# Optimization experiments

Hardware: AMD Instinct MI355X
Metric: run time of the kernel (lower is better)

Reference implementation:

```python
import jax, jax.numpy as jnp
import numpy as np

ALPHA_MIN = 1e-6
SN_EPS = 1e-6


def _spectral_normalize(W, u):
    # One power iteration (torch spectral_norm, n_power_iterations=1).
    v = W.T @ u
    v = v / (jnp.linalg.norm(v) + SN_EPS)
    u1 = W @ v
    u1 = u1 / (jnp.linalg.norm(u1) + SN_EPS)
    u1 = jax.lax.stop_gradient(u1)
    v = jax.lax.stop_gradient(v)
    sigma = u1 @ (W @ v)
    return W / sigma


def setup_inputs() -> dict:
    key = jax.random.key(0)
    ks = jax.random.split(key, 11)
    B, T, D, K = 32, 2048, 512, 128
    x = jax.random.normal(ks[0], (B, T, D), jnp.float32)
    dt = jax.random.uniform(ks[1], (B, T), jnp.float32)
    alpha_mod = jax.random.normal(ks[2], (B, T, K), jnp.float32)
    omega_mod = jax.random.normal(ks[3], (B, T, K), jnp.float32)
    tau_mod = jax.random.normal(ks[4], (B, T, 1), jnp.float32)
    s_real_raw = jax.random.normal(ks[5], (K,), jnp.float32)
    s_imag = jax.random.normal(ks[6], (K,), jnp.float32)
    tau_raw = jax.random.normal(ks[7], (1,), jnp.float32)
    W_orig = jax.random.normal(ks[8], (K, D), jnp.float32) * (1.0 / np.sqrt(D))
    b = jax.random.normal(ks[9], (K,), jnp.float32) * 0.01
    u_sn = jax.random.normal(ks[10], (K,), jnp.float32)
    u_sn = u_sn / jnp.linalg.norm(u_sn)
    return {"x": x, "dt": dt, "alpha_mod": alpha_mod, "omega_mod": omega_mod,
            "tau_mod": tau_mod, "s_real_raw": s_real_raw, "s_imag": s_imag,
            "tau_raw": tau_raw, "W_orig": W_orig, "b": b, "u_sn": u_sn}


def reference(x, dt, alpha_mod, omega_mod, tau_mod, s_real_raw, s_imag,
              tau_raw, W_orig, b, u_sn):
    B, T, D = x.shape
    K = W_orig.shape[0]

    # global timescale and poles
    tau = jax.nn.softplus(tau_raw[0]) + 1e-3
    alpha0 = (jax.nn.softplus(s_real_raw) + ALPHA_MIN) * tau  # [K]
    omega0 = s_imag * tau                                      # [K]

    # time-varying modulation (all log-scale)
    scale = jnp.exp(tau_mod)                                   # [B,T,1]
    alpha = alpha0 * jnp.exp(alpha_mod) * scale                # [B,T,K]
    omega = omega0 * jnp.exp(omega_mod) * scale                # [B,T,K]

    dt3 = dt[..., None]                                        # [B,T,1]
    rho = jnp.exp(-alpha * dt3)                                # [B,T,K]
    theta = omega * dt3
    cos_t = jnp.cos(theta)
    sin_t = jnp.sin(theta)

    # spectral-norm projection u = x @ W_sn^T + b -> [B,T,K]
    W_sn = _spectral_normalize(W_orig, u_sn)
    u = jnp.einsum('btd,kd->btk', x, W_sn) + b

    # complex recurrence: z_t = rho_t * e^{i theta_t} * z_{t-1} + u_t
    def step(carry, inp):
        c, s = carry
        rt, ct, st, ut = inp
        c_new = rt * (c * ct - s * st) + ut
        s_new = rt * (c * st + s * ct)
        return (c_new, s_new), (c_new, s_new)

    xs = (jnp.swapaxes(rho, 0, 1), jnp.swapaxes(cos_t, 0, 1),
          jnp.swapaxes(sin_t, 0, 1), jnp.swapaxes(u, 0, 1))  # [T,B,K]
    init = (jnp.zeros((B, K), u.dtype), jnp.zeros((B, K), u.dtype))
    _, (C, S) = jax.lax.scan(step, init, xs)
    C = jnp.swapaxes(C, 0, 1)  # [B,T,K]
    S = jnp.swapaxes(S, 0, 1)
    return jnp.concatenate([C, S], axis=-1)  # [B,T,2K]
```

## Files before the change

### kernel.cpp

```cpp
#include <hip/hip_runtime.h>
#include <hip/hip_bf16.h>
#include <math.h>

typedef __bf16 bf16x8 __attribute__((ext_vector_type(8)));
typedef float f32x4 __attribute__((ext_vector_type(4)));

#define B_SZ 32
#define T_SZ 2048
#define D_SZ 512
#define K_SZ 128
#define TC 32
#define NC 64

__device__ __forceinline__ float softplus_f(float x){
  return x > 20.f ? x : log1pf(expf(x));
}

__global__ __launch_bounds__(512) void sn_prep(const float* __restrict__ W,
                                               const float* __restrict__ u_sn,
                                               __bf16* __restrict__ Wb){
  __shared__ float red[512];
  __shared__ float vsh[512];
  __shared__ float ush[128];
  const int t = threadIdx.x;
  if (t < 128) ush[t] = u_sn[t];
  __syncthreads();
  float t1 = 0.f;
  for (int k = 0; k < K_SZ; ++k) t1 += W[k*D_SZ + t] * ush[k];
  red[t] = t1 * t1;
  __syncthreads();
  for (int s = 256; s > 0; s >>= 1){ if (t < s) red[t] += red[t+s]; __syncthreads(); }
  const float n1 = sqrtf(red[0]);
  vsh[t] = t1 / (n1 + 1e-6f);
  __syncthreads();
  float t2 = 0.f;
  if (t < 128){
    const float* Wr = W + (size_t)t * D_SZ;
    for (int d = 0; d < D_SZ; ++d) t2 += Wr[d] * vsh[d];
  }
  __syncthreads();
  red[t] = (t < 128) ? t2*t2 : 0.f;
  __syncthreads();
  for (int s = 256; s > 0; s >>= 1){ if (t < s) red[t] += red[t+s]; __syncthreads(); }
  const float n2sq = red[0];
  const float sigma = n2sq / (sqrtf(n2sq) + 1e-6f);
  const float inv = 1.f / sigma;
  for (int i = t; i < K_SZ*D_SZ; i += 512) Wb[i] = (__bf16)(W[i] * inv);
}

__global__ __launch_bounds__(256) void gemm_xw(const float* __restrict__ X,
                                               const __bf16* __restrict__ Wb,
                                               float* __restrict__ U){
  __shared__ bf16x8 As[1024];
  __shared__ bf16x8 Bs[1024];
  const int tid = threadIdx.x;
  const int lane = tid & 63;
  const int wid = tid >> 6;
  const int wm = wid >> 1, wn = wid & 1;
  const int rowbase = blockIdx.x * 128;
  const int L15 = lane & 15, Lq = lane >> 4;
  f32x4 acc[4][4] = {};

  for (int kk = 0; kk < D_SZ; kk += 64){
    #pragma unroll
    for (int r = 0; r < 4; ++r){
      const int c = tid + 256*r;
      const int L = c & 63, fb = c >> 6;
      const int i = fb >> 1, s = fb & 1;
      const int row = i*16 + (L & 15);
      const int gcol = kk + s*32 + ((L >> 4) << 3);
      const float4* p = (const float4*)(X + (size_t)(rowbase + row)*D_SZ + gcol);
      const float4 v0 = p[0], v1 = p[1];
      bf16x8 f;
      f[0]=(__bf16)v0.x; f[1]=(__bf16)v0.y; f[2]=(__bf16)v0.z; f[3]=(__bf16)v0.w;
      f[4]=(__bf16)v1.x; f[5]=(__bf16)v1.y; f[6]=(__bf16)v1.z; f[7]=(__bf16)v1.w;
      As[c] = f;
      Bs[c] = *(const bf16x8*)(Wb + (size_t)row*D_SZ + gcol);
    }
    __syncthreads();
    #pragma unroll
    for (int s = 0; s < 2; ++s){
      bf16x8 af[4], bfr[4];
      #pragma unroll
      for (int ii = 0; ii < 4; ++ii) af[ii]  = As[((wm*4+ii)*2 + s)*64 + lane];
      #pragma unroll
      for (int jj = 0; jj < 4; ++jj) bfr[jj] = Bs[((wn*4+jj)*2 + s)*64 + lane];
      #pragma unroll
      for (int ii = 0; ii < 4; ++ii)
        #pragma unroll
        for (int jj = 0; jj < 4; ++jj)
          acc[ii][jj] = __builtin_amdgcn_mfma_f32_16x16x32_bf16(af[ii], bfr[jj], acc[ii][jj], 0, 0, 0);
    }
    __syncthreads();
  }
  #pragma unroll
  for (int ii = 0; ii < 4; ++ii){
    const int m = rowbase + (wm*4+ii)*16 + (Lq << 2);
    #pragma unroll
    for (int jj = 0; jj < 4; ++jj){
      const int n = (wn*4+jj)*16 + L15;
      #pragma unroll
      for (int r = 0; r < 4; ++r)
        U[(size_t)(m + r)*K_SZ + n] = acc[ii][jj][r];
    }
  }
}

__global__ __launch_bounds__(128) void pass_a(
    const float* __restrict__ alpha_mod, const float* __restrict__ omega_mod,
    const float* __restrict__ Uarr, const float* __restrict__ dt,
    const float* __restrict__ tau_mod, const float* __restrict__ s_real,
    const float* __restrict__ s_imag, const float* __restrict__ tau_raw,
    const float* __restrict__ bvec,
    float* __restrict__ sumA, float* __restrict__ sumT,
    float* __restrict__ Zr, float* __restrict__ Zi){
  const int k = threadIdx.x;
  const int c = blockIdx.x, b = blockIdx.y;
  const float tau = softplus_f(tau_raw[0]) + 1e-3f;
  const float a0 = (softplus_f(s_real[k]) + 1e-6f) * tau;
  const float w0 = s_imag[k] * tau;
  const float bk = bvec[k];
  __shared__ float sdt[TC], ssc[TC];
  const int t0 = c * TC;
  if (k < TC) sdt[k] = dt[b*T_SZ + t0 + k];
  else if (k < 2*TC) ssc[k-TC] = __expf(tau_mod[b*T_SZ + t0 + k - TC]);
  __syncthreads();
  float zr = 0.f, zs = 0.f, sA = 0.f, sT = 0.f;
  const size_t base = ((size_t)(b*T_SZ + t0))*K_SZ + k;
  #pragma unroll 4
  for (int i = 0; i < TC; ++i){
    const float am = alpha_mod[base + (size_t)i*K_SZ];
    const float om = omega_mod[base + (size_t)i*K_SZ];
    const float uu = Uarr[base + (size_t)i*K_SZ] + bk;
    const float scdt = ssc[i] * sdt[i];
    const float ad = a0 * __expf(am) * scdt;
    const float th = w0 * __expf(om) * scdt;
    const float rho = __expf(-ad);
    float st, ct; __sincosf(th, &st, &ct);
    const float nr = rho*(zr*ct - zs*st) + uu;
    const float ns = rho*(zr*st + zs*ct);
    zr = nr; zs = ns;
    sA += ad; sT += th;
  }
  const size_t idx = ((size_t)(b*NC + c))*K_SZ + k;
  sumA[idx] = sA; sumT[idx] = sT; Zr[idx] = zr; Zi[idx] = zs;
}

__global__ __launch_bounds__(256) void pass_b(
    const float* __restrict__ sumA, const float* __restrict__ sumT,
    const float* __restrict__ Zr, const float* __restrict__ Zi,
    float* __restrict__ Cr, float* __restrict__ Ci){
  const int id = blockIdx.x*256 + threadIdx.x;
  const int b = id >> 7, k = id & 127;
  float er = 0.f, ei = 0.f;
  #pragma unroll 8
  for (int c = 0; c < NC; ++c){
    const size_t idx = ((size_t)(b*NC + c))*K_SZ + k;
    Cr[idx] = er; Ci[idx] = ei;
    const float rho = __expf(-sumA[idx]);
    float st, ct; __sincosf(sumT[idx], &st, &ct);
    const float ar = rho*ct, ai = rho*st;
    const float nr = Zr[idx] + ar*er - ai*ei;
    const float ni = Zi[idx] + ar*ei + ai*er;
    er = nr; ei = ni;
  }
}

__global__ __launch_bounds__(128) void pass_c(
    const float* __restrict__ alpha_mod, const float* __restrict__ omega_mod,
    const float* __restrict__ Uarr, const float* __restrict__ dt,
    const float* __restrict__ tau_mod, const float* __restrict__ s_real,
    const float* __restrict__ s_imag, const float* __restrict__ tau_raw,
    const float* __restrict__ bvec,
    const float* __restrict__ Cr, const float* __restrict__ Ci,
    float* __restrict__ out){
  const int k = threadIdx.x;
  const int c = blockIdx.x, b = blockIdx.y;
  const float tau = softplus_f(tau_raw[0]) + 1e-3f;
  const float a0 = (softplus_f(s_real[k]) + 1e-6f) * tau;
  const float w0 = s_imag[k] * tau;
  const float bk = bvec[k];
  __shared__ float sdt[TC], ssc[TC];
  const int t0 = c * TC;
  if (k < TC) sdt[k] = dt[b*T_SZ + t0 + k];
  else if (k < 2*TC) ssc[k-TC] = __expf(tau_mod[b*T_SZ + t0 + k - TC]);
  __syncthreads();
  const size_t cidx = ((size_t)(b*NC + c))*K_SZ + k;
  float zr = Cr[cidx], zs = Ci[cidx];
  const size_t base = ((size_t)(b*T_SZ + t0))*K_SZ + k;
  const size_t obase = ((size_t)(b*T_SZ + t0))*(2*K_SZ) + k;
  #pragma unroll 4
  for (int i = 0; i < TC; ++i){
    const float am = alpha_mod[base + (size_t)i*K_SZ];
    const float om = omega_mod[base + (size_t)i*K_SZ];
    const float uu = Uarr[base + (size_t)i*K_SZ] + bk;
    const float scdt = ssc[i] * sdt[i];
    const float ad = a0 * __expf(am) * scdt;
    const float th = w0 * __expf(om) * scdt;
    const float rho = __expf(-ad);
    float st, ct; __sincosf(th, &st, &ct);
    const float nr = rho*(zr*ct - zs*st) + uu;
    const float ns = rho*(zr*st + zs*ct);
    zr = nr; zs = ns;
    out[obase + (size_t)i*(2*K_SZ)] = zr;
    out[obase + (size_t)i*(2*K_SZ) + K_SZ] = zs;
  }
}

extern "C" void kernel_launch(void* const* d_in, const int* in_sizes, int n_in,
                              void* d_out, int out_size, void* d_ws, size_t ws_size,
                              hipStream_t stream){
  (void)in_sizes; (void)n_in; (void)out_size; (void)ws_size;
  const float* x         = (const float*)d_in[0];
  const float* dt        = (const float*)d_in[1];
  const float* alpha_mod = (const float*)d_in[2];
  const float* omega_mod = (const float*)d_in[3];
  const float* tau_mod   = (const float*)d_in[4];
  const float* s_real    = (const float*)d_in[5];
  const float* s_imag    = (const float*)d_in[6];
  const float* tau_raw   = (const float*)d_in[7];
  const float* W         = (const float*)d_in[8];
  const float* bvec      = (const float*)d_in[9];
  const float* u_sn      = (const float*)d_in[10];
  float* out = (float*)d_out;

  char* w = (char*)d_ws;
  __bf16* Wb = (__bf16*)w;
  float* U   = (float*)(w + 131072);
  size_t off = 131072 + (size_t)B_SZ*T_SZ*K_SZ*4;
  const size_t SUMN = (size_t)B_SZ*NC*K_SZ*4;
  float* sumA = (float*)(w + off); off += SUMN;
  float* sumT = (float*)(w + off); off += SUMN;
  float* Zr   = (float*)(w + off); off += SUMN;
  float* Zi   = (float*)(w + off); off += SUMN;
  float* Cr   = (float*)(w + off); off += SUMN;
  float* Ci   = (float*)(w + off); off += SUMN;

  sn_prep<<<1, 512, 0, stream>>>(W, u_sn, Wb);
  gemm_xw<<<(B_SZ*T_SZ)/128, 256, 0, stream>>>(x, Wb, U);
  pass_a<<<dim3(NC, B_SZ), 128, 0, stream>>>(alpha_mod, omega_mod, U, dt, tau_mod,
                                             s_real, s_imag, tau_raw, bvec,
                                             sumA, sumT, Zr, Zi);
  pass_b<<<16, 256, 0, stream>>>(sumA, sumT, Zr, Zi, Cr, Ci);
  pass_c<<<dim3(NC, B_SZ), 128, 0, stream>>>(alpha_mod, omega_mod, U, dt, tau_mod,
                                             s_real, s_imag, tau_raw, bvec,
                                             Cr, Ci, out);
}
```

Measured before the change: 336.0 us.

## Store projection in bf16, vectorize scan passes and GEMM loads

The GEMM output U is now stored as bf16 instead of fp32, halving the intermediate traffic that both scan passes read. The scan passes and pass_b now handle two channels per thread with float2/bf16x2 accesses, and each block covers four chunks. GEMM global loads are remapped so each thread reads contiguous columns of one row. The spectral-norm prep is also vectorized with float4. Rounding U to bf16 adds precision loss on the recurrence input, and pass_b now launches fewer threads, which lowers its parallelism.

New measurement: 340.0 us. No clear change (+1.2%).

```diff
diff --git a/kernel.cpp b/kernel.cpp
--- a/kernel.cpp
+++ b/kernel.cpp
@@ -3,6 +3,8 @@
 #include <math.h>
 
 typedef __bf16 bf16x8 __attribute__((ext_vector_type(8)));
+typedef __bf16 bf16x4 __attribute__((ext_vector_type(4)));
+typedef __bf16 bf16x2 __attribute__((ext_vector_type(2)));
 typedef float f32x4 __attribute__((ext_vector_type(4)));
 
 #define B_SZ 32
@@ -26,6 +28,7 @@
   if (t < 128) ush[t] = u_sn[t];
   __syncthreads();
   float t1 = 0.f;
+  #pragma unroll 8
   for (int k = 0; k < K_SZ; ++k) t1 += W[k*D_SZ + t] * ush[k];
   red[t] = t1 * t1;
   __syncthreads();
@@ -35,8 +38,13 @@
   __syncthreads();
   float t2 = 0.f;
   if (t < 128){
-    const float* Wr = W + (size_t)t * D_SZ;
-    for (int d = 0; d < D_SZ; ++d) t2 += Wr[d] * vsh[d];
+    const float4* Wr = (const float4*)(W + (size_t)t * D_SZ);
+    const float4* vp = (const float4*)vsh;
+    #pragma unroll 8
+    for (int d = 0; d < D_SZ/4; ++d){
+      const float4 a = Wr[d], v = vp[d];
+      t2 += a.x*v.x + a.y*v.y + a.z*v.z + a.w*v.w;
+    }
   }
   __syncthreads();
   red[t] = (t < 128) ? t2*t2 : 0.f;
@@ -45,12 +53,17 @@
   const float n2sq = red[0];
   const float sigma = n2sq / (sqrtf(n2sq) + 1e-6f);
   const float inv = 1.f / sigma;
-  for (int i = t; i < K_SZ*D_SZ; i += 512) Wb[i] = (__bf16)(W[i] * inv);
+  for (int i = t; i < K_SZ*D_SZ/4; i += 512){
+    const float4 v = ((const float4*)W)[i];
+    bf16x4 o; o[0]=(__bf16)(v.x*inv); o[1]=(__bf16)(v.y*inv);
+    o[2]=(__bf16)(v.z*inv); o[3]=(__bf16)(v.w*inv);
+    ((bf16x4*)Wb)[i] = o;
+  }
 }
 
 __global__ __launch_bounds__(256) void gemm_xw(const float* __restrict__ X,
                                                const __bf16* __restrict__ Wb,
-                                               float* __restrict__ U){
+                                               __bf16* __restrict__ U){
   __shared__ bf16x8 As[1024];
   __shared__ bf16x8 Bs[1024];
   const int tid = threadIdx.x;
@@ -64,18 +77,17 @@
   for (int kk = 0; kk < D_SZ; kk += 64){
     #pragma unroll
     for (int r = 0; r < 4; ++r){
-      const int c = tid + 256*r;
-      const int L = c & 63, fb = c >> 6;
-      const int i = fb >> 1, s = fb & 1;
-      const int row = i*16 + (L & 15);
-      const int gcol = kk + s*32 + ((L >> 4) << 3);
-      const float4* p = (const float4*)(X + (size_t)(rowbase + row)*D_SZ + gcol);
+      const int fc = tid + 256*r;
+      const int row = fc >> 3, cg = fc & 7;
+      const float4* p = (const float4*)(X + (size_t)(rowbase + row)*D_SZ + kk + cg*8);
       const float4 v0 = p[0], v1 = p[1];
       bf16x8 f;
       f[0]=(__bf16)v0.x; f[1]=(__bf16)v0.y; f[2]=(__bf16)v0.z; f[3]=(__bf16)v0.w;
       f[4]=(__bf16)v1.x; f[5]=(__bf16)v1.y; f[6]=(__bf16)v1.z; f[7]=(__bf16)v1.w;
-      As[c] = f;
-      Bs[c] = *(const bf16x8*)(Wb + (size_t)row*D_SZ + gcol);
+      const int fb = ((row >> 4) << 1) | (cg >> 2);
+      const int ll = (row & 15) | ((cg & 3) << 4);
+      As[fb*64 + ll] = f;
+      Bs[fb*64 + ll] = *(const bf16x8*)(Wb + (size_t)row*D_SZ + kk + cg*8);
     }
     __syncthreads();
     #pragma unroll
@@ -101,109 +113,155 @@
       const int n = (wn*4+jj)*16 + L15;
       #pragma unroll
       for (int r = 0; r < 4; ++r)
-        U[(size_t)(m + r)*K_SZ + n] = acc[ii][jj][r];
-    }
-  }
-}
-
-__global__ __launch_bounds__(128) void pass_a(
+        U[(size_t)(m + r)*K_SZ + n] = (__bf16)acc[ii][jj][r];
+    }
+  }
+}
+
+__global__ __launch_bounds__(256) void pass_a(
     const float* __restrict__ alpha_mod, const float* __restrict__ omega_mod,
-    const float* __restrict__ Uarr, const float* __restrict__ dt,
+    const __bf16* __restrict__ Uarr, const float* __restrict__ dt,
     const float* __restrict__ tau_mod, const float* __restrict__ s_real,
     const float* __restrict__ s_imag, const float* __restrict__ tau_raw,
     const float* __restrict__ bvec,
-    float* __restrict__ sumA, float* __restrict__ sumT,
-    float* __restrict__ Zr, float* __restrict__ Zi){
-  const int k = threadIdx.x;
-  const int c = blockIdx.x, b = blockIdx.y;
+    float2* __restrict__ sumA, float2* __restrict__ sumT,
+    float2* __restrict__ Zr, float2* __restrict__ Zi){
+  const int t = threadIdx.x;
+  const int kh = t & 63;
+  const int cl = t >> 6;
+  const int b = blockIdx.y;
+  const int c = blockIdx.x*4 + cl;
+  const int t0 = c * TC;
+  __shared__ float sdt[4*TC], ssc[4*TC];
+  if (t < 128){
+    const int tg = blockIdx.x*4*TC + t;
+    sdt[t] = dt[b*T_SZ + tg];
+    ssc[t] = __expf(tau_mod[b*T_SZ + tg]);
+  }
+  __syncthreads();
   const float tau = softplus_f(tau_raw[0]) + 1e-3f;
-  const float a0 = (softplus_f(s_real[k]) + 1e-6f) * tau;
-  const float w0 = s_imag[k] * tau;
-  const float bk = bvec[k];
-  __shared__ float sdt[TC], ssc[TC];
-  const int t0 = c * TC;
-  if (k < TC) sdt[k] = dt[b*T_SZ + t0 + k];
-  else if (k < 2*TC) ssc[k-TC] = __expf(tau_mod[b*T_SZ + t0 + k - TC]);
-  __syncthreads();
-  float zr = 0.f, zs = 0.f, sA = 0.f, sT = 0.f;
-  const size_t base = ((size_t)(b*T_SZ + t0))*K_SZ + k;
+  const float2 sr = ((const float2*)s_real)[kh];
+  const float2 si = ((const float2*)s_imag)[kh];
+  const float2 bk = ((const float2*)bvec)[kh];
+  const float a0[2] = {(softplus_f(sr.x)+1e-6f)*tau, (softplus_f(sr.y)+1e-6f)*tau};
+  const float w0[2] = {si.x*tau, si.y*tau};
+  float zr[2]={0,0}, zs[2]={0,0}, sA[2]={0,0}, sT[2]={0,0};
+  const float* sd = sdt + cl*TC;
+  const float* ss = ssc + cl*TC;
+  const size_t row = (size_t)(b*T_SZ + t0);
+  const float2* amp = (const float2*)(alpha_mod + row*K_SZ) + kh;
+  const float2* omp = (const float2*)(omega_mod + row*K_SZ) + kh;
+  const bf16x2* up  = (const bf16x2*)(Uarr + row*K_SZ) + kh;
   #pragma unroll 4
   for (int i = 0; i < TC; ++i){
-    const float am = alpha_mod[base + (size_t)i*K_SZ];
-    const float om = omega_mod[base + (size_t)i*K_SZ];
-    const float uu = Uarr[base + (size_t)i*K_SZ] + bk;
-    const float scdt = ssc[i] * sdt[i];
-    const float ad = a0 * __expf(am) * scdt;
-    const float th = w0 * __expf(om) * scdt;
-    const float rho = __expf(-ad);
-    float st, ct; __sincosf(th, &st, &ct);
-    const float nr = rho*(zr*ct - zs*st) + uu;
-    const float ns = rho*(zr*st + zs*ct);
-    zr = nr; zs = ns;
-    sA += ad; sT += th;
-  }
-  const size_t idx = ((size_t)(b*NC + c))*K_SZ + k;
-  sumA[idx] = sA; sumT[idx] = sT; Zr[idx] = zr; Zi[idx] = zs;
+    const float2 am = amp[(size_t)i*64];
+    const float2 om = omp[(size_t)i*64];
+    const bf16x2 u2 = up[(size_t)i*64];
+    const float scdt = ss[i] * sd[i];
+    #pragma unroll
+    for (int j = 0; j < 2; ++j){
+      const float ad = a0[j] * __expf(j ? am.y : am.x) * scdt;
+      const float th = w0[j] * __expf(j ? om.y : om.x) * scdt;
+      const float rho = __expf(-ad);
+      float st, ct; __sincosf(th, &st, &ct);
+      const float uu = (float)u2[j] + (j ? bk.y : bk.x);
+      const float nr = rho*(zr[j]*ct - zs[j]*st) + uu;
+      const float ns = rho*(zr[j]*st + zs[j]*ct);
+      zr[j] = nr; zs[j] = ns;
+      sA[j] += ad; sT[j] += th;
+    }
+  }
+  const size_t idx = ((size_t)(b*NC + c))*64 + kh;
+  sumA[idx] = make_float2(sA[0], sA[1]);
+  sumT[idx] = make_float2(sT[0], sT[1]);
+  Zr[idx]   = make_float2(zr[0], zr[1]);
+  Zi[idx]   = make_float2(zs[0], zs[1]);
 }
 
 __global__ __launch_bounds__(256) void pass_b(
-    const float* __restrict__ sumA, const float* __restrict__ sumT,
-    const float* __restrict__ Zr, const float* __restrict__ Zi,
-    float* __restrict__ Cr, float* __restrict__ Ci){
+    const float2* __restrict__ sumA, const float2* __restrict__ sumT,
+    const float2* __restrict__ Zr, const float2* __restrict__ Zi,
+    float2* __restrict__ Cr, float2* __restrict__ Ci){
   const int id = blockIdx.x*256 + threadIdx.x;
-  const int b = id >> 7, k = id & 127;
-  float er = 0.f, ei = 0.f;
-  #pragma unroll 8
+  const int b = id >> 6, kh = id & 63;
+  float er[2]={0,0}, ei[2]={0,0};
+  #pragma unroll 4
   for (int c = 0; c < NC; ++c){
-    const size_t idx = ((size_t)(b*NC + c))*K_SZ + k;
-    Cr[idx] = er; Ci[idx] = ei;
-    const float rho = __expf(-sumA[idx]);
-    float st, ct; __sincosf(sumT[idx], &st, &ct);
-    const float ar = rho*ct, ai = rho*st;
-    const float nr = Zr[idx] + ar*er - ai*ei;
-    const float ni = Zi[idx] + ar*ei + ai*er;
-    er = nr; ei = ni;
-  }
-}
-
-__global__ __launch_bounds__(128) void pass_c(
+    const size_t idx = ((size_t)(b*NC + c))*64 + kh;
+    Cr[idx] = make_float2(er[0], er[1]);
+    Ci[idx] = make_float2(ei[0], ei[1]);
+    const float2 sa = sumA[idx], st4 = sumT[idx];
+    const float2 zr = Zr[idx],   zi  = Zi[idx];
+    #pragma unroll
+    for (int j = 0; j < 2; ++j){
+      const float rho = __expf(-(j ? sa.y : sa.x));
+      float st, ct; __sincosf(j ? st4.y : st4.x, &st, &ct);
+      const float ar = rho*ct, ai = rho*st;
+      const float zrj = j ? zr.y : zr.x, zij = j ? zi.y : zi.x;
+      const float nr = zrj + ar*er[j] - ai*ei[j];
+      const float ni = zij + ar*ei[j] + ai*er[j];
+      er[j] = nr; ei[j] = ni;
+    }
+  }
+}
+
+__global__ __launch_bounds__(256) void pass_c(
     const float* __restrict__ alpha_mod, const float* __restrict__ omega_mod,
-    const float* __restrict__ Uarr, const float* __restrict__ dt,
+    const __bf16* __restrict__ Uarr, const float* __restrict__ dt,
     const float* __restrict__ tau_mod, const float* __restrict__ s_real,
     const float* __restrict__ s_imag, const float* __restrict__ tau_raw,
     const float* __restrict__ bvec,
-    const float* __restrict__ Cr, const float* __restrict__ Ci,
+    const float2* __restrict__ Cr, const float2* __restrict__ Ci,
     float* __restrict__ out){
-  const int k = threadIdx.x;
-  const int c = blockIdx.x, b = blockIdx.y;
+  const int t = threadIdx.x;
+  const int kh = t & 63;
+  const int cl = t >> 6;
+  const int b = blockIdx.y;
+  const int c = blockIdx.x*4 + cl;
+  const int t0 = c * TC;
+  __shared__ float sdt[4*TC], ssc[4*TC];
+  if (t < 128){
+    const int tg = blockIdx.x*4*TC + t;
+    sdt[t] = dt[b*T_SZ + tg];
+    ssc[t] = __expf(tau_mod[b*T_SZ + tg]);
+  }
+  __syncthreads();
   const float tau = softplus_f(tau_raw[0]) + 1e-3f;
-  const float a0 = (softplus_f(s_real[k]) + 1e-6f) * tau;
-  const float w0 = s_imag[k] * tau;
-  const float bk = bvec[k];
-  __shared__ float sdt[TC], ssc[TC];
-  const int t0 = c * TC;
-  if (k < TC) sdt[k] = dt[b*T_SZ + t0 + k];
-  else if (k < 2*TC) ssc[k-TC] = __expf(tau_mod[b*T_SZ + t0 + k - TC]);
-  __syncthreads();
-  const size_t cidx = ((size_t)(b*NC + c))*K_SZ + k;
-  float zr = Cr[cidx], zs = Ci[cidx];
-  const size_t base = ((size_t)(b*T_SZ + t0))*K_SZ + k;
-  const size_t obase = ((size_t)(b*T_SZ + t0))*(2*K_SZ) + k;
+  const float2 sr = ((const float2*)s_real)[kh];
+  const float2 si = ((const float2*)s_imag)[kh];
+  const float2 bk = ((const float2*)bvec)[kh];
+  const float a0[2] = {(softplus_f(sr.x)+1e-6f)*tau, (softplus_f(sr.y)+1e-6f)*tau};
+  const float w0[2] = {si.x*tau, si.y*tau};
+  const size_t cidx = ((size_t)(b*NC + c))*64 + kh;
+  const float2 cr = Cr[cidx], cim = Ci[cidx];
+  float zr[2] = {cr.x, cr.y}, zs[2] = {cim.x, cim.y};
+  const float* sd = sdt + cl*TC;
+  const float* ss = ssc + cl*TC;
+  const size_t row = (size_t)(b*T_SZ + t0);
+  const float2* amp = (const float2*)(alpha_mod + row*K_SZ) + kh;
+  const float2* omp = (const float2*)(omega_mod + row*K_SZ) + kh;
+  const bf16x2* up  = (const bf16x2*)(Uarr + row*K_SZ) + kh;
+  float2* outC = (float2*)(out + row*(2*K_SZ)) + kh;
+  float2* outS = outC + 64;
   #pragma unroll 4
   for (int i = 0; i < TC; ++i){
-    const float am = alpha_mod[base + (size_t)i*K_SZ];
-    const float om = omega_mod[base + (size_t)i*K_SZ];
-    const float uu = Uarr[base + (size_t)i*K_SZ] + bk;
-    const float scdt = ssc[i] * sdt[i];
-    const float ad = a0 * __expf(am) * scdt;
-    const float th = w0 * __expf(om) * scdt;
-    const float rho = __expf(-ad);
-    float st, ct; __sincosf(th, &st, &ct);
-    const float nr = rho*(zr*ct - zs*st) + uu;
-    const float ns = rho*(zr*st + zs*ct);
-    zr = nr; zs = ns;
-    out[obase + (size_t)i*(2*K_SZ)] = zr;
-    out[obase + (size_t)i*(2*K_SZ) + K_SZ] = zs;
+    const float2 am = amp[(size_t)i*64];
+    const float2 om = omp[(size_t)i*64];
+    const bf16x2 u2 = up[(size_t)i*64];
+    const float scdt = ss[i] * sd[i];
+    #pragma unroll
+    for (int j = 0; j < 2; ++j){
+      const float ad = a0[j] * __expf(j ? am.y : am.x) * scdt;
+      const float th = w0[j] * __expf(j ? om.y : om.x) * scdt;
+      const float rho = __expf(-ad);
+      float st, ct; __sincosf(th, &st, &ct);
+      const float uu = (float)u2[j] + (j ? bk.y : bk.x);
+      const float nr = rho*(zr[j]*ct - zs[j]*st) + uu;
+      const float ns = rho*(zr[j]*st + zs[j]*ct);
+      zr[j] = nr; zs[j] = ns;
+    }
+    outC[(size_t)i*128] = make_float2(zr[0], zr[1]);
+    outS[(size_t)i*128] = make_float2(zs[0], zs[1]);
   }
 }
 
@@ -226,23 +284,23 @@
 
   char* w = (char*)d_ws;
   __bf16* Wb = (__bf16*)w;
-  float* U   = (float*)(w + 131072);
-  size_t off = 131072 + (size_t)B_SZ*T_SZ*K_SZ*4;
+  __bf16* U  = (__bf16*)(w + 131072);
+  size_t off = 131072 + (size_t)B_SZ*T_SZ*K_SZ*2;
   const size_t SUMN = (size_t)B_SZ*NC*K_SZ*4;
-  float* sumA = (float*)(w + off); off += SUMN;
-  float* sumT = (float*)(w + off); off += SUMN;
-  float* Zr   = (float*)(w + off); off += SUMN;
-  float* Zi   = (float*)(w + off); off += SUMN;
-  float* Cr   = (float*)(w + off); off += SUMN;
-  float* Ci   = (float*)(w + off); off += SUMN;
+  float2* sumA = (float2*)(w + off); off += SUMN;
+  float2* sumT = (float2*)(w + off); off += SUMN;
+  float2* Zr   = (float2*)(w + off); off += SUMN;
+  float2* Zi   = (float2*)(w + off); off += SUMN;
+  float2* Cr   = (float2*)(w + off); off += SUMN;
+  float2* Ci   = (float2*)(w + off); off += SUMN;
 
   sn_prep<<<1, 512, 0, stream>>>(W, u_sn, Wb);
   gemm_xw<<<(B_SZ*T_SZ)/128, 256, 0, stream>>>(x, Wb, U);
-  pass_a<<<dim3(NC, B_SZ), 128, 0, stream>>>(alpha_mod, omega_mod, U, dt, tau_mod,
-                                             s_real, s_imag, tau_raw, bvec,
-                                             sumA, sumT, Zr, Zi);
-  pass_b<<<16, 256, 0, stream>>>(sumA, sumT, Zr, Zi, Cr, Ci);
-  pass_c<<<dim3(NC, B_SZ), 128, 0, stream>>>(alpha_mod, omega_mod, U, dt, tau_mod,
-                                             s_real, s_imag, tau_raw, bvec,
-                                             Cr, Ci, out);
-}
+  pass_a<<<dim3(NC/4, B_SZ), 256, 0, stream>>>(alpha_mod, omega_mod, U, dt, tau_mod,
+                                               s_real, s_imag, tau_raw, bvec,
+                                               sumA, sumT, Zr, Zi);
+  pass_b<<<8, 256, 0, stream>>>(sumA, sumT, Zr, Zi, Cr, Ci);
+  pass_c<<<dim3(NC/4, B_SZ), 256, 0, stream>>>(alpha_mod, omega_mod, U, dt, tau_mod,
+                                               s_real, s_imag, tau_raw, bvec,
+                                               Cr, Ci, out);
+}
```
